# Kernel tuning notes

Hardware: AMD Instinct MI355X
Metric: run time of the kernel (lower is better)

Reference implementation:

```python
import jax, jax.numpy as jnp
import numpy as np

LN_EPS = 1e-12


def _layernorm(x, gamma, beta):
    mu = jnp.mean(x, axis=-1, keepdims=True)
    var = jnp.mean((x - mu) ** 2, axis=-1, keepdims=True)
    return (x - mu) * jax.lax.rsqrt(var + LN_EPS) * gamma + beta


def _gcn(x, node_emb, time_emb, wpool, bpool, ln_g, ln_b):
    # x: [B,N,C]; node_emb: [N,D]; time_emb: [D]
    e = _layernorm(node_emb + time_emb[None, :], ln_g, ln_b)          # [N,D] (dropout in eval = identity)
    adj = jax.nn.softmax(e @ e.T, axis=1)                             # [N,N] dynamic adjacency
    weights = jnp.einsum('nd,dkio->nkio', e, wpool)                   # [N,2,Cin,Cout] per-node weights
    bias = e @ bpool                                                  # [N,Cout]
    # supports = [I, adj]: identity support is just x itself
    x_g = jnp.stack([x, jnp.einsum('nm,bmc->bnc', adj, x)], axis=2)   # [B,N,2,Cin]
    return jnp.einsum('bnki,nkio->bno', x_g, weights) + bias          # [B,N,Cout]


def setup_inputs() -> dict:
    key = jax.random.key(0)
    ks = jax.random.split(key, 10)
    B, N, Cin, H, D = 32, 2048, 32, 64, 64
    s = 0.1
    return {
        'x': jax.random.normal(ks[0], (B, N, Cin), jnp.float32),
        'state': jax.random.normal(ks[1], (B, N, H), jnp.float32),
        'node_embeddings': jax.random.normal(ks[2], (N, D), jnp.float32),
        'time_embeddings': jax.random.normal(ks[3], (D,), jnp.float32),
        'gate_wpool': jax.random.normal(ks[4], (D, 2, Cin + H, 2 * H), jnp.float32) * s,
        'gate_bpool': jax.random.normal(ks[5], (D, 2 * H), jnp.float32) * s,
        'gate_ln_g': jnp.ones((D,), jnp.float32),
        'gate_ln_b': jnp.zeros((D,), jnp.float32),
        'update_wpool': jax.random.normal(ks[6], (D, 2, Cin + H, H), jnp.float32) * s,
        'update_bpool': jax.random.normal(ks[7], (D, H), jnp.float32) * s,
        'update_ln_g': jnp.ones((D,), jnp.float32),
        'update_ln_b': jnp.zeros((D,), jnp.float32),
    }


def reference(x, state, node_embeddings, time_embeddings,
              gate_wpool, gate_bpool, gate_ln_g, gate_ln_b,
              update_wpool, update_bpool, update_ln_g, update_ln_b):
    H = state.shape[-1]
    inp = jnp.concatenate([x, state], axis=-1)                        # [B,N,Cin+H]
    z_r = jax.nn.sigmoid(_gcn(inp, node_embeddings, time_embeddings,
                              gate_wpool, gate_bpool, gate_ln_g, gate_ln_b))
    z, r = z_r[..., :H], z_r[..., H:]
    cand = jnp.concatenate([x, z * state], axis=-1)
    hc = jnp.tanh(_gcn(cand, node_embeddings, time_embeddings,
                       update_wpool, update_bpool, update_ln_g, update_ln_b))
    return r * state + (1.0 - r) * hc
```

## Files before the change

kernel.cpp:

```cpp
#include <hip/hip_runtime.h>

typedef _Float16 f16;
typedef _Float16 half8 __attribute__((ext_vector_type(8)));
typedef float f32x4 __attribute__((ext_vector_type(4)));

#define NN 2048
#define BB 32
#define CINC 32
#define HH 64
#define DD 64
#define C1 96
#define KI 192
#define OG 128
#define OU 64
#define WCG 24576
#define WCU 12288

#define XGI(n, ks, b, kk) (((((size_t)(n)) * 6 + (ks)) * BB + (b)) * 32 + (kk))

__device__ __forceinline__ f32x4 mfma16(half8 a, half8 b, f32x4 c) {
  return __builtin_amdgcn_mfma_f32_16x16x32_f16(a, b, c, 0, 0, 0);
}

typedef __attribute__((address_space(1))) const void* gas_t;
typedef __attribute__((address_space(3))) void* las_t;
__device__ __forceinline__ void gl_lds16(const void* g, void* l) {
  __builtin_amdgcn_global_load_lds((gas_t)g, (las_t)l, 16, 0, 0);
}

#define SWZ(row, kb) (((row) << 7) + ((kb) ^ (((row) & 7) << 4)))

__global__ __launch_bounds__(256) void k_ln_bias(
    const float* __restrict__ ne, const float* __restrict__ te,
    const float* __restrict__ gg, const float* __restrict__ gb,
    const float* __restrict__ ug, const float* __restrict__ ub,
    const float* __restrict__ gbp, const float* __restrict__ ubp,
    f16* __restrict__ egh, f16* __restrict__ euh,
    float* __restrict__ biasg, float* __restrict__ biasu) {
  __shared__ float esg[4][64];
  __shared__ float esu[4][64];
  int nl = threadIdx.x >> 6;
  int node = blockIdx.x * 4 + nl;
  int d = threadIdx.x & 63;
  float v = ne[node * DD + d] + te[d];
  float s = v;
  #pragma unroll
  for (int m = 1; m < 64; m <<= 1) s += __shfl_xor(s, m, 64);
  float mu = s * (1.f / 64.f);
  float df = v - mu;
  float q = df * df;
  #pragma unroll
  for (int m = 1; m < 64; m <<= 1) q += __shfl_xor(q, m, 64);
  float rs = rsqrtf(q * (1.f / 64.f) + 1e-12f);
  float base = df * rs;
  float a = base * gg[d] + gb[d];
  float b = base * ug[d] + ub[d];
  egh[node * DD + d] = (f16)a;
  euh[node * DD + d] = (f16)b;
  esg[nl][d] = a; esu[nl][d] = b;
  __syncthreads();
  #pragma unroll
  for (int i = 0; i < 3; ++i) {
    int u = i * 256 + threadIdx.x;
    int un = u / 192, oo = u % 192;
    int n2 = blockIdx.x * 4 + un;
    float acc = 0.f;
    if (oo < OG) {
      #pragma unroll 8
      for (int dd = 0; dd < 64; ++dd) acc += esg[un][dd] * gbp[dd * OG + oo];
      biasg[(size_t)n2 * OG + oo] = acc;
    } else {
      int o = oo - OG;
      #pragma unroll 8
      for (int dd = 0; dd < 64; ++dd) acc += esu[un][dd] * ubp[dd * OU + o];
      biasu[(size_t)n2 * OU + o] = acc;
    }
  }
}

__global__ __launch_bounds__(256) void k_wpool_t(const float* __restrict__ gwp,
                                                 const float* __restrict__ uwp,
                                                 f16* __restrict__ wtg,
                                                 f16* __restrict__ wtu) {
  const int upd = blockIdx.z;
  if (upd && blockIdx.y >= OU / 16) return;
  const float* wpool = upd ? uwp : gwp;
  f16* wt = upd ? wtu : wtg;
  const int O = upd ? OU : OG;
  __shared__ float tile[64][17];
  int ki = blockIdx.x;
  int o0 = blockIdx.y * 16;
  int t = threadIdx.x;
  const int ks = ki >> 5, kk = ki & 31;
  #pragma unroll
  for (int i = 0; i < 4; ++i) {
    int e2 = i * 256 + t;
    int d = e2 >> 4, o = e2 & 15;
    tile[d][o] = wpool[((size_t)d * KI + ki) * O + o0 + o];
  }
  __syncthreads();
  #pragma unroll
  for (int i = 0; i < 4; ++i) {
    int e2 = i * 256 + t;
    int o = e2 >> 6, d = e2 & 63;
    size_t row = ((size_t)ks * O + (o0 + o)) * 32 + kk;
    wt[row * DD + d] = (f16)tile[d][o];
  }
}

__global__ __launch_bounds__(256) void k_build_inp(const float* __restrict__ x,
                                                   const float* __restrict__ st,
                                                   f16* __restrict__ cm,
                                                   f16* __restrict__ xg,
                                                   f16* __restrict__ sth) {
  __shared__ f16 tile[96][66];
  int mb = blockIdx.x * 64;
  int b = blockIdx.y;
  int t = threadIdx.x;
  #pragma unroll
  for (int i = 0; i < 24; ++i) {
    int e2 = i * 256 + t;
    int m = e2 / 96, c = e2 % 96;
    float v = (c < CINC) ? x[((size_t)b * NN + mb + m) * CINC + c]
                         : st[((size_t)b * NN + mb + m) * HH + c - CINC];
    f16 h = (f16)v;
    tile[c][m] = h;
    xg[XGI(mb + m, c >> 5, b, c & 31)] = h;
    if (c >= CINC) sth[((size_t)b * NN + mb + m) * HH + c - CINC] = h;
  }
  __syncthreads();
  #pragma unroll
  for (int i = 0; i < 24; ++i) {
    int e2 = i * 256 + t;
    int c = e2 >> 6, m = e2 & 63;
    cm[((size_t)b * C1 + c) * NN + mb + m] = tile[c][m];
  }
}

__global__ __launch_bounds__(256) void k_transpose_zs(const f16* __restrict__ zs,
                                                      f16* __restrict__ cm) {
  __shared__ f16 tile[64][66];
  int mb = blockIdx.x * 64;
  int b = blockIdx.y;
  int t = threadIdx.x;
  #pragma unroll
  for (int i = 0; i < 16; ++i) {
    int e2 = i * 256 + t;
    int m = e2 >> 6, o = e2 & 63;
    tile[o][m] = zs[((size_t)b * NN + mb + m) * HH + o];
  }
  __syncthreads();
  #pragma unroll
  for (int i = 0; i < 16; ++i) {
    int e2 = i * 256 + t;
    int o = e2 >> 6, m = e2 & 63;
    cm[((size_t)b * C1 + CINC + o) * NN + mb + m] = tile[o][m];
  }
}

__global__ __launch_bounds__(256) void k_attn(const f16* __restrict__ eh,
                                              f16* __restrict__ adj) {
  const int r0 = blockIdx.x * 16;
  const int w = threadIdx.x >> 6, lane = threadIdx.x & 63;
  const int fr = lane & 15, fq = lane >> 4;
  __shared__ float pm[4][16], ps[4][16];
  __shared__ float fm[16], fs[16];
  const half8 a0 = *(const half8*)&eh[(size_t)(r0 + fr) * DD + fq * 8];
  const half8 a1 = *(const half8*)&eh[(size_t)(r0 + fr) * DD + 32 + fq * 8];
  float m[4], s[4];
  #pragma unroll
  for (int r = 0; r < 4; ++r) { m[r] = -3.0e38f; s[r] = 0.f; }
  for (int ct = 0; ct < 32; ++ct) {
    const int c0 = w * 512 + ct * 16;
    half8 b0 = *(const half8*)&eh[(size_t)(c0 + fr) * DD + fq * 8];
    half8 b1 = *(const half8*)&eh[(size_t)(c0 + fr) * DD + 32 + fq * 8];
    f32x4 d = mfma16(a0, b0, f32x4{0.f, 0.f, 0.f, 0.f});
    d = mfma16(a1, b1, d);
    #pragma unroll
    for (int r = 0; r < 4; ++r) {
      float mn = fmaxf(m[r], d[r]);
      s[r] = s[r] * __expf(m[r] - mn) + __expf(d[r] - mn);
      m[r] = mn;
    }
  }
  #pragma unroll
  for (int r = 0; r < 4; ++r) {
    #pragma unroll
    for (int mk = 1; mk < 16; mk <<= 1) {
      float mo = __shfl_xor(m[r], mk, 64);
      float so = __shfl_xor(s[r], mk, 64);
      float mn = fmaxf(m[r], mo);
      s[r] = s[r] * __expf(m[r] - mn) + so * __expf(mo - mn);
      m[r] = mn;
    }
  }
  if (fr == 0) {
    #pragma unroll
    for (int r = 0; r < 4; ++r) { pm[w][fq * 4 + r] = m[r]; ps[w][fq * 4 + r] = s[r]; }
  }
  __syncthreads();
  if (threadIdx.x < 16) {
    float M = -3.0e38f;
    #pragma unroll
    for (int i = 0; i < 4; ++i) M = fmaxf(M, pm[i][threadIdx.x]);
    float S = 0.f;
    #pragma unroll
    for (int i = 0; i < 4; ++i) S += ps[i][threadIdx.x] * __expf(pm[i][threadIdx.x] - M);
    fm[threadIdx.x] = M; fs[threadIdx.x] = 1.f / S;
  }
  __syncthreads();
  float Mr[4], Sr[4];
  #pragma unroll
  for (int r = 0; r < 4; ++r) { Mr[r] = fm[fq * 4 + r]; Sr[r] = fs[fq * 4 + r]; }
  for (int ct = 0; ct < 32; ++ct) {
    const int c0 = w * 512 + ct * 16;
    half8 b0 = *(const half8*)&eh[(size_t)(c0 + fr) * DD + fq * 8];
    half8 b1 = *(const half8*)&eh[(size_t)(c0 + fr) * DD + 32 + fq * 8];
    f32x4 d = mfma16(a0, b0, f32x4{0.f, 0.f, 0.f, 0.f});
    d = mfma16(a1, b1, d);
    #pragma unroll
    for (int r = 0; r < 4; ++r)
      adj[(size_t)(r0 + fq * 4 + r) * NN + c0 + fr] = (f16)(__expf(d[r] - Mr[r]) * Sr[r]);
  }
}

#define BM 64
#define BN 96

__global__ __launch_bounds__(256, 4) void k_gemm_xa(const f16* __restrict__ A,
                                                    const f16* __restrict__ Bm,
                                                    f16* __restrict__ xg) {
  const int orig = blockIdx.x;
  const int xcd = orig & 7, j = orig >> 3;
  const int nb = (j >> 2) * BM;
  const int by = (xcd << 2) + (j & 3);
  const int cb = by * BN;
  const int tid = threadIdx.x;
  const int w = tid >> 6, lane = tid & 63;
  const int wr = (w >> 1) * 32, wc = (w & 1) * 48;
  const int fr = lane & 15, fq = lane >> 4;

  const int arow = tid >> 3;
  const int acolb = ((tid & 7) * 16) ^ ((arow & 7) << 4);
  const char* asrc = (const char*)A + (size_t)(nb + arow) * (NN * 2) + acolb;
  const char* bsrc = (const char*)Bm + (size_t)(cb + arow) * (NN * 2) + acolb;

  __shared__ f16 Al[2][BM * 64];
  __shared__ f16 Bl[2][BN * 64];
  auto stage = [&](int buf, int kt) {
    const size_t ko = (size_t)kt * 2;
    char* ad = (char*)&Al[buf][0] + (w << 10);
    char* bd = (char*)&Bl[buf][0] + (w << 10);
    gl_lds16(asrc + ko, ad);
    gl_lds16(asrc + ko + (size_t)32 * (NN * 2), ad + 4096);
    gl_lds16(bsrc + ko, bd);
    gl_lds16(bsrc + ko + (size_t)32 * (NN * 2), bd + 4096);
    gl_lds16(bsrc + ko + (size_t)64 * (NN * 2), bd + 8192);
  };

  f32x4 acc[2][3] = {};
  stage(0, 0);
  for (int kt = 0; kt < NN; kt += 64) {
    const int cur = (kt >> 6) & 1;
    if (kt + 64 < NN) {
      stage(cur ^ 1, kt + 64);
      asm volatile("s_waitcnt vmcnt(5)" ::: "memory");
    } else {
      asm volatile("s_waitcnt vmcnt(0)" ::: "memory");
    }
    __builtin_amdgcn_sched_barrier(0);
    __builtin_amdgcn_s_barrier();
    const char* Ab = (const char*)&Al[cur][0];
    const char* Bb = (const char*)&Bl[cur][0];
    half8 af[2][2], bf[2][3];
    #pragma unroll
    for (int k0 = 0; k0 < 2; ++k0) {
      const int kb = k0 * 64 + fq * 16;
      #pragma unroll
      for (int mt = 0; mt < 2; ++mt)
        af[k0][mt] = *(const half8*)(Ab + SWZ(wr + mt * 16 + fr, kb));
      #pragma unroll
      for (int nt = 0; nt < 3; ++nt)
        bf[k0][nt] = *(const half8*)(Bb + SWZ(wc + nt * 16 + fr, kb));
    }
    asm volatile("s_waitcnt lgkmcnt(0)" ::: "memory");
    __builtin_amdgcn_sched_barrier(0);
    __builtin_amdgcn_s_barrier();
    #pragma unroll
    for (int k0 = 0; k0 < 2; ++k0)
      #pragma unroll
      for (int mt = 0; mt < 2; ++mt)
        #pragma unroll
        for (int nt = 0; nt < 3; ++nt)
          acc[mt][nt] = mfma16(af[k0][mt], bf[k0][nt], acc[mt][nt]);
  }
  #pragma unroll
  for (int mt = 0; mt < 2; ++mt)
    #pragma unroll
    for (int nt = 0; nt < 3; ++nt)
      #pragma unroll
      for (int r = 0; r < 4; ++r) {
        int n = nb + wr + mt * 16 + fq * 4 + r;
        int l = wc + nt * 16 + fr;
        xg[XGI(n, 3 + (l >> 5), by, l & 31)] = (f16)acc[mt][nt][r];
      }
}

__global__ __launch_bounds__(256) void k_gemm_w2(const f16* __restrict__ A,
                                                 const f16* __restrict__ B,
                                                 f16* __restrict__ W, int ncols) {
  __shared__ f16 Al[128 * 64];
  __shared__ f16 Bl[128 * 64];
  const int cb = blockIdx.x * 128;
  const int nb = blockIdx.y * 128;
  const int tid = threadIdx.x;
  const int w = tid >> 6, lane = tid & 63;
  const int wr = (w >> 1) * 64, wc = (w & 1) * 64;
  const int fr = lane & 15, fq = lane >> 4;
  const int arow = tid >> 3;
  const int acolb = ((tid & 7) * 16) ^ ((arow & 7) << 4);
  const char* asrc = (const char*)A + (size_t)(nb + arow) * 128 + acolb;
  const char* bsrc = (const char*)B + (size_t)(cb + arow) * 128 + acolb;
  char* ad = (char*)Al + (w << 10);
  char* bd = (char*)Bl + (w << 10);
  #pragma unroll
  for (int j = 0; j < 4; ++j) gl_lds16(asrc + (size_t)j * 32 * 128, ad + j * 4096);
  #pragma unroll
  for (int j = 0; j < 4; ++j) gl_lds16(bsrc + (size_t)j * 32 * 128, bd + j * 4096);
  __syncthreads();
  f32x4 acc[4][4] = {};
  #pragma unroll
  for (int k0 = 0; k0 < 2; ++k0) {
    const int kb = k0 * 64 + fq * 16;
    half8 af[4], bf[4];
    #pragma unroll
    for (int mt = 0; mt < 4; ++mt)
      af[mt] = *(const half8*)((const char*)Al + SWZ(wr + mt * 16 + fr, kb));
    #pragma unroll
    for (int nt = 0; nt < 4; ++nt)
      bf[nt] = *(const half8*)((const char*)Bl + SWZ(wc + nt * 16 + fr, kb));
    #pragma unroll
    for (int mt = 0; mt < 4; ++mt)
      #pragma unroll
      for (int nt = 0; nt < 4; ++nt)
        acc[mt][nt] = mfma16(af[mt], bf[nt], acc[mt][nt]);
  }
  #pragma unroll
  for (int mt = 0; mt < 4; ++mt)
    #pragma unroll
    for (int nt = 0; nt < 4; ++nt)
      #pragma unroll
      for (int r = 0; r < 4; ++r) {
        int n = nb + wr + mt * 16 + fq * 4 + r;
        int c = cb + wc + nt * 16 + fr;
        W[(size_t)n * ncols + c] = (f16)acc[mt][nt][r];
      }
}

template <bool GATE>
__global__ __launch_bounds__(256) void k_apply3(
    const f16* __restrict__ xg, const f16* __restrict__ W,
    const float* __restrict__ bias,
    const f16* __restrict__ sth,
    f16* xgw, f16* __restrict__ zs, f16* __restrict__ rbuf,
    float* __restrict__ outp) {
  constexpr int O = GATE ? OG : OU;
  constexpr int WS = GATE ? WCG : WCU;
  constexpr int NOT_ = GATE ? 2 : 1;
  const int n = blockIdx.x;
  const int lane = threadIdx.x & 63, w = threadIdx.x >> 6;
  const int fr = lane & 15, fq = lane >> 4;
  half8 af[2][6];
  #pragma unroll
  for (int mt = 0; mt < 2; ++mt) {
    #pragma unroll
    for (int ks = 0; ks < 6; ++ks)
      af[mt][ks] = *(const half8*)&xg[XGI(n, ks, mt * 16 + fr, fq * 8)];
  }
  if (GATE) __syncthreads();
  half8 bf[6][NOT_];
  #pragma unroll
  for (int ks = 0; ks < 6; ++ks) {
    #pragma unroll
    for (int ot = 0; ot < NOT_; ++ot) {
      int o = (GATE ? (w * 2 + ot) : w) * 16 + fr;
      bf[ks][ot] = *(const half8*)&W[(size_t)n * WS + (((size_t)ks * O + o) << 5) + fq * 8];
    }
  }
  f32x4 acc[2][NOT_] = {};
  #pragma unroll
  for (int ks = 0; ks < 6; ++ks)
    #pragma unroll
    for (int ot = 0; ot < NOT_; ++ot)
      #pragma unroll
      for (int mt = 0; mt < 2; ++mt)
        acc[mt][ot] = mfma16(af[mt][ks], bf[ks][ot], acc[mt][ot]);
  #pragma unroll
  for (int mt = 0; mt < 2; ++mt)
    #pragma unroll
    for (int ot = 0; ot < NOT_; ++ot) {
      const int o = (GATE ? (w * 2 + ot) : w) * 16 + fr;
      const float bs = bias[(size_t)n * O + o];
      #pragma unroll
      for (int r = 0; r < 4; ++r) {
        int b = mt * 16 + fq * 4 + r;
        float val = acc[mt][ot][r] + bs;
        if (GATE) {
          float s = 1.f / (1.f + expf(-val));
          if (o < HH) {
            size_t bno = ((size_t)b * NN + n) * HH + o;
            float zst = s * (float)sth[bno];
            xgw[XGI(n, 1 + (o >> 5), b, o & 31)] = (f16)zst;
            zs[bno] = (f16)zst;
          } else {
            rbuf[((size_t)b * NN + n) * HH + (o - HH)] = (f16)s;
          }
        } else {
          size_t bno = ((size_t)b * NN + n) * HH + o;
          float hc = tanhf(val);
          float rr = (float)rbuf[bno];
          outp[bno] = rr * (float)sth[bno] + (1.f - rr) * hc;
        }
      }
    }
}

extern "C" void kernel_launch(void* const* d_in, const int* in_sizes, int n_in,
                              void* d_out, int out_size, void* d_ws, size_t ws_size,
                              hipStream_t stream) {
  const float* x   = (const float*)d_in[0];
  const float* st  = (const float*)d_in[1];
  const float* ne  = (const float*)d_in[2];
  const float* te  = (const float*)d_in[3];
  const float* gwp = (const float*)d_in[4];
  const float* gbp = (const float*)d_in[5];
  const float* gg  = (const float*)d_in[6];
  const float* gb  = (const float*)d_in[7];
  const float* uwp = (const float*)d_in[8];
  const float* ubp = (const float*)d_in[9];
  const float* ug  = (const float*)d_in[10];
  const float* ub  = (const float*)d_in[11];
  float* out = (float*)d_out;

  char* wsb = (char*)d_ws;
  size_t off = 0;
  auto alloc = [&](size_t bytes) {
    char* p = wsb + off;
    off = (off + bytes + 255) & ~(size_t)255;
    return p;
  };
  f16*   egh   = (f16*)  alloc((size_t)NN * DD * 2);
  f16*   euh   = (f16*)  alloc((size_t)NN * DD * 2);
  float* biasg = (float*)alloc((size_t)NN * OG * 4);
  float* biasu = (float*)alloc((size_t)NN * OU * 4);
  f16*   wtg   = (f16*)  alloc((size_t)WCG * DD * 2);
  f16*   wtu   = (f16*)  alloc((size_t)WCU * DD * 2);
  f16*   xg    = (f16*)  alloc((size_t)NN * BB * KI * 2);
  f16*   cm    = (f16*)  alloc((size_t)BB * C1 * NN * 2);
  f16*   zs    = (f16*)  alloc((size_t)BB * NN * HH * 2);
  f16*   rbuf  = (f16*)  alloc((size_t)BB * NN * HH * 2);
  f16*   sth   = (f16*)  alloc((size_t)BB * NN * HH * 2);
  f16*   adj   = (f16*)  alloc((size_t)NN * NN * 2);
  f16*   W     = (f16*)  alloc((size_t)NN * WCG * 2);
  (void)ws_size; (void)in_sizes; (void)n_in; (void)out_size;

  hipLaunchKernelGGL(k_ln_bias, dim3(NN / 4), dim3(256), 0, stream,
                     ne, te, gg, gb, ug, ub, gbp, ubp,
                     egh, euh, biasg, biasu);
  hipLaunchKernelGGL(k_wpool_t, dim3(KI, OG / 16, 2), dim3(256), 0, stream,
                     gwp, uwp, wtg, wtu);
  hipLaunchKernelGGL(k_build_inp, dim3(NN / 64, BB), dim3(256), 0, stream,
                     x, st, cm, xg, sth);

  hipLaunchKernelGGL(k_attn, dim3(NN / 16), dim3(256), 0, stream, egh, adj);
  hipLaunchKernelGGL(k_gemm_xa, dim3(1024), dim3(256), 0, stream, adj, cm, xg);
  hipLaunchKernelGGL(k_gemm_w2, dim3(WCG / 128, NN / 128), dim3(256), 0, stream,
                     egh, wtg, W, WCG);
  hipLaunchKernelGGL((k_apply3<true>), dim3(NN), dim3(256), 0, stream,
                     xg, W, biasg, sth, xg, zs, rbuf, (float*)nullptr);
  hipLaunchKernelGGL(k_transpose_zs, dim3(NN / 64, BB), dim3(256), 0, stream, zs, cm);

  hipLaunchKernelGGL(k_attn, dim3(NN / 16), dim3(256), 0, stream, euh, adj);
  hipLaunchKernelGGL(k_gemm_xa, dim3(1024), dim3(256), 0, stream, adj, cm, xg);
  hipLaunchKernelGGL(k_gemm_w2, dim3(WCU / 128, NN / 128), dim3(256), 0, stream,
                     euh, wtu, W, WCU);
  hipLaunchKernelGGL((k_apply3<false>), dim3(NN), dim3(256), 0, stream,
                     xg, W, biasu, sth, (f16*)nullptr, (f16*)nullptr, rbuf, out);
}
```

Baseline: 222.5 us.

## Re-layout xg and per-node weights into 8-element segments and stage via LDS DMA

```diff
diff --git a/kernel.cpp b/kernel.cpp
--- a/kernel.cpp
+++ b/kernel.cpp
@@ -16,7 +16,8 @@
 #define WCG 24576
 #define WCU 12288
 
-#define XGI(n, ks, b, kk) (((((size_t)(n)) * 6 + (ks)) * BB + (b)) * 32 + (kk))
+#define XGI(n, ks, b, kk) \
+  ((((((size_t)(n)) * 6 + (ks)) * 4 + ((kk) >> 3)) * BB + (b)) * 8 + ((kk) & 7))
 
 __device__ __forceinline__ f32x4 mfma16(half8 a, half8 b, f32x4 c) {
   return __builtin_amdgcn_mfma_f32_16x16x32_f16(a, b, c, 0, 0, 0);
@@ -91,7 +92,8 @@
   int ki = blockIdx.x;
   int o0 = blockIdx.y * 16;
   int t = threadIdx.x;
-  const int ks = ki >> 5, kk = ki & 31;
+  const int seg = (ki >> 5) * 4 + ((ki >> 3) & 3);
+  const int kkl = ki & 7;
   #pragma unroll
   for (int i = 0; i < 4; ++i) {
     int e2 = i * 256 + t;
@@ -103,7 +105,7 @@
   for (int i = 0; i < 4; ++i) {
     int e2 = i * 256 + t;
     int o = e2 >> 6, d = e2 & 63;
-    size_t row = ((size_t)ks * O + (o0 + o)) * 32 + kk;
+    size_t row = ((size_t)seg * O + (o0 + o)) * 8 + kkl;
     wt[row * DD + d] = (f16)tile[d][o];
   }
 }
@@ -358,43 +360,47 @@
 }
 
 template <bool GATE>
-__global__ __launch_bounds__(256) void k_apply3(
+__global__ __launch_bounds__(256, GATE ? 2 : 4) void k_apply4(
     const f16* __restrict__ xg, const f16* __restrict__ W,
     const float* __restrict__ bias,
     const f16* __restrict__ sth,
     f16* xgw, f16* __restrict__ zs, f16* __restrict__ rbuf,
     float* __restrict__ outp) {
   constexpr int O = GATE ? OG : OU;
-  constexpr int WS = GATE ? WCG : WCU;
+  constexpr int WB = O * KI * 2;
+  constexpr int XB = KI * BB * 2;
   constexpr int NOT_ = GATE ? 2 : 1;
+  __shared__ __align__(128) char lds[WB + XB];
   const int n = blockIdx.x;
-  const int lane = threadIdx.x & 63, w = threadIdx.x >> 6;
+  const int tid = threadIdx.x;
+  const int w = tid >> 6, lane = tid & 63;
   const int fr = lane & 15, fq = lane >> 4;
-  half8 af[2][6];
-  #pragma unroll
-  for (int mt = 0; mt < 2; ++mt) {
-    #pragma unroll
-    for (int ks = 0; ks < 6; ++ks)
-      af[mt][ks] = *(const half8*)&xg[XGI(n, ks, mt * 16 + fr, fq * 8)];
-  }
-  if (GATE) __syncthreads();
-  half8 bf[6][NOT_];
+
+  const char* wsrc = (const char*)W + (size_t)n * WB + tid * 16;
+  const char* xsrc = (const char*)xg + (size_t)n * XB + tid * 16;
+  char* wdst = lds + (w << 10);
+  char* xdst = lds + WB + (w << 10);
+  #pragma unroll
+  for (int j = 0; j < WB / 4096; ++j) gl_lds16(wsrc + j * 4096, wdst + j * 4096);
+  #pragma unroll
+  for (int j = 0; j < XB / 4096; ++j) gl_lds16(xsrc + j * 4096, xdst + j * 4096);
+  __syncthreads();
+
+  const char* xl = lds + WB;
+  f32x4 acc[2][NOT_] = {};
   #pragma unroll
   for (int ks = 0; ks < 6; ++ks) {
+    const int seg = (ks * 4 + fq);
+    half8 af0 = *(const half8*)(xl + (seg * 32 + fr) * 16);
+    half8 af1 = *(const half8*)(xl + (seg * 32 + 16 + fr) * 16);
     #pragma unroll
     for (int ot = 0; ot < NOT_; ++ot) {
-      int o = (GATE ? (w * 2 + ot) : w) * 16 + fr;
-      bf[ks][ot] = *(const half8*)&W[(size_t)n * WS + (((size_t)ks * O + o) << 5) + fq * 8];
-    }
-  }
-  f32x4 acc[2][NOT_] = {};
-  #pragma unroll
-  for (int ks = 0; ks < 6; ++ks)
-    #pragma unroll
-    for (int ot = 0; ot < NOT_; ++ot)
-      #pragma unroll
-      for (int mt = 0; mt < 2; ++mt)
-        acc[mt][ot] = mfma16(af[mt][ks], bf[ks][ot], acc[mt][ot]);
+      const int o = (GATE ? (w * 2 + ot) : w) * 16 + fr;
+      half8 bf = *(const half8*)(lds + (seg * O + o) * 16);
+      acc[0][ot] = mfma16(af0, bf, acc[0][ot]);
+      acc[1][ot] = mfma16(af1, bf, acc[1][ot]);
+    }
+  }
   #pragma unroll
   for (int mt = 0; mt < 2; ++mt)
     #pragma unroll
@@ -476,7 +482,7 @@
   hipLaunchKernelGGL(k_gemm_xa, dim3(1024), dim3(256), 0, stream, adj, cm, xg);
   hipLaunchKernelGGL(k_gemm_w2, dim3(WCG / 128, NN / 128), dim3(256), 0, stream,
                      egh, wtg, W, WCG);
-  hipLaunchKernelGGL((k_apply3<true>), dim3(NN), dim3(256), 0, stream,
+  hipLaunchKernelGGL((k_apply4<true>), dim3(NN), dim3(256), 0, stream,
                      xg, W, biasg, sth, xg, zs, rbuf, (float*)nullptr);
   hipLaunchKernelGGL(k_transpose_zs, dim3(NN / 64, BB), dim3(256), 0, stream, zs, cm);
 
@@ -484,6 +490,6 @@
   hipLaunchKernelGGL(k_gemm_xa, dim3(1024), dim3(256), 0, stream, adj, cm, xg);
   hipLaunchKernelGGL(k_gemm_w2, dim3(WCU / 128, NN / 128), dim3(256), 0, stream,
                      euh, wtu, W, WCU);
-  hipLaunchKernelGGL((k_apply3<false>), dim3(NN), dim3(256), 0, stream,
+  hipLaunchKernelGGL((k_apply4<false>), dim3(NN), dim3(256), 0, stream,
                      xg, W, biasu, sth, (f16*)nullptr, (f16*)nullptr, rbuf, out);
 }
```

Measured after the change: 239.5 us. 1.08x slower.

## Merge prep kernels into one launch and batch both attention passes

Applied to the files above, without the earlier changes.

```diff
diff --git a/kernel.cpp b/kernel.cpp
--- a/kernel.cpp
+++ b/kernel.cpp
@@ -17,6 +17,7 @@
 #define WCU 12288
 
 #define XGI(n, ks, b, kk) (((((size_t)(n)) * 6 + (ks)) * BB + (b)) * 32 + (kk))
+#define STHI(n, b, o) ((((size_t)(n)) * BB + (b)) * HH + (o))
 
 __device__ __forceinline__ f32x4 mfma16(half8 a, half8 b, f32x4 c) {
   return __builtin_amdgcn_mfma_f32_16x16x32_f16(a, b, c, 0, 0, 0);
@@ -30,110 +31,108 @@
 
 #define SWZ(row, kb) (((row) << 7) + ((kb) ^ (((row) & 7) << 4)))
 
-__global__ __launch_bounds__(256) void k_ln_bias(
+__global__ __launch_bounds__(256) void k_prep(
     const float* __restrict__ ne, const float* __restrict__ te,
     const float* __restrict__ gg, const float* __restrict__ gb,
     const float* __restrict__ ug, const float* __restrict__ ub,
     const float* __restrict__ gbp, const float* __restrict__ ubp,
+    const float* __restrict__ gwp, const float* __restrict__ uwp,
+    const float* __restrict__ x, const float* __restrict__ st,
     f16* __restrict__ egh, f16* __restrict__ euh,
-    float* __restrict__ biasg, float* __restrict__ biasu) {
-  __shared__ float esg[4][64];
-  __shared__ float esu[4][64];
-  int nl = threadIdx.x >> 6;
-  int node = blockIdx.x * 4 + nl;
-  int d = threadIdx.x & 63;
-  float v = ne[node * DD + d] + te[d];
-  float s = v;
-  #pragma unroll
-  for (int m = 1; m < 64; m <<= 1) s += __shfl_xor(s, m, 64);
-  float mu = s * (1.f / 64.f);
-  float df = v - mu;
-  float q = df * df;
-  #pragma unroll
-  for (int m = 1; m < 64; m <<= 1) q += __shfl_xor(q, m, 64);
-  float rs = rsqrtf(q * (1.f / 64.f) + 1e-12f);
-  float base = df * rs;
-  float a = base * gg[d] + gb[d];
-  float b = base * ug[d] + ub[d];
-  egh[node * DD + d] = (f16)a;
-  euh[node * DD + d] = (f16)b;
-  esg[nl][d] = a; esu[nl][d] = b;
-  __syncthreads();
-  #pragma unroll
-  for (int i = 0; i < 3; ++i) {
-    int u = i * 256 + threadIdx.x;
-    int un = u / 192, oo = u % 192;
-    int n2 = blockIdx.x * 4 + un;
-    float acc = 0.f;
-    if (oo < OG) {
-      #pragma unroll 8
-      for (int dd = 0; dd < 64; ++dd) acc += esg[un][dd] * gbp[dd * OG + oo];
-      biasg[(size_t)n2 * OG + oo] = acc;
-    } else {
-      int o = oo - OG;
-      #pragma unroll 8
-      for (int dd = 0; dd < 64; ++dd) acc += esu[un][dd] * ubp[dd * OU + o];
-      biasu[(size_t)n2 * OU + o] = acc;
-    }
-  }
-}
-
-__global__ __launch_bounds__(256) void k_wpool_t(const float* __restrict__ gwp,
-                                                 const float* __restrict__ uwp,
-                                                 f16* __restrict__ wtg,
-                                                 f16* __restrict__ wtu) {
-  const int upd = blockIdx.z;
-  if (upd && blockIdx.y >= OU / 16) return;
-  const float* wpool = upd ? uwp : gwp;
-  f16* wt = upd ? wtu : wtg;
-  const int O = upd ? OU : OG;
-  __shared__ float tile[64][17];
-  int ki = blockIdx.x;
-  int o0 = blockIdx.y * 16;
-  int t = threadIdx.x;
-  const int ks = ki >> 5, kk = ki & 31;
-  #pragma unroll
-  for (int i = 0; i < 4; ++i) {
-    int e2 = i * 256 + t;
-    int d = e2 >> 4, o = e2 & 15;
-    tile[d][o] = wpool[((size_t)d * KI + ki) * O + o0 + o];
-  }
-  __syncthreads();
-  #pragma unroll
-  for (int i = 0; i < 4; ++i) {
-    int e2 = i * 256 + t;
-    int o = e2 >> 6, d = e2 & 63;
-    size_t row = ((size_t)ks * O + (o0 + o)) * 32 + kk;
-    wt[row * DD + d] = (f16)tile[d][o];
-  }
-}
-
-__global__ __launch_bounds__(256) void k_build_inp(const float* __restrict__ x,
-                                                   const float* __restrict__ st,
-                                                   f16* __restrict__ cm,
-                                                   f16* __restrict__ xg,
-                                                   f16* __restrict__ sth) {
-  __shared__ f16 tile[96][66];
-  int mb = blockIdx.x * 64;
-  int b = blockIdx.y;
-  int t = threadIdx.x;
-  #pragma unroll
-  for (int i = 0; i < 24; ++i) {
-    int e2 = i * 256 + t;
-    int m = e2 / 96, c = e2 % 96;
-    float v = (c < CINC) ? x[((size_t)b * NN + mb + m) * CINC + c]
-                         : st[((size_t)b * NN + mb + m) * HH + c - CINC];
-    f16 h = (f16)v;
-    tile[c][m] = h;
-    xg[XGI(mb + m, c >> 5, b, c & 31)] = h;
-    if (c >= CINC) sth[((size_t)b * NN + mb + m) * HH + c - CINC] = h;
-  }
-  __syncthreads();
-  #pragma unroll
-  for (int i = 0; i < 24; ++i) {
-    int e2 = i * 256 + t;
-    int c = e2 >> 6, m = e2 & 63;
-    cm[((size_t)b * C1 + c) * NN + mb + m] = tile[c][m];
+    float* __restrict__ biasg, float* __restrict__ biasu,
+    f16* __restrict__ wtg, f16* __restrict__ wtu,
+    f16* __restrict__ cm, f16* __restrict__ xg, f16* __restrict__ sth) {
+  __shared__ __align__(16) char smem[12672];
+  const int bid = blockIdx.x;
+  const int t = threadIdx.x;
+  if (bid < 512) {
+    float (*esg)[64] = (float(*)[64])smem;
+    float (*esu)[64] = (float(*)[64])(smem + 1024);
+    int nl = t >> 6;
+    int node = bid * 4 + nl;
+    int d = t & 63;
+    float v = ne[node * DD + d] + te[d];
+    float s = v;
+    #pragma unroll
+    for (int m = 1; m < 64; m <<= 1) s += __shfl_xor(s, m, 64);
+    float mu = s * (1.f / 64.f);
+    float df = v - mu;
+    float q = df * df;
+    #pragma unroll
+    for (int m = 1; m < 64; m <<= 1) q += __shfl_xor(q, m, 64);
+    float rs = rsqrtf(q * (1.f / 64.f) + 1e-12f);
+    float base = df * rs;
+    float a = base * gg[d] + gb[d];
+    float b = base * ug[d] + ub[d];
+    egh[node * DD + d] = (f16)a;
+    euh[node * DD + d] = (f16)b;
+    esg[nl][d] = a; esu[nl][d] = b;
+    __syncthreads();
+    #pragma unroll
+    for (int i = 0; i < 3; ++i) {
+      int u = i * 256 + t;
+      int un = u / 192, oo = u % 192;
+      int n2 = bid * 4 + un;
+      float acc = 0.f;
+      if (oo < OG) {
+        #pragma unroll 8
+        for (int dd = 0; dd < 64; ++dd) acc += esg[un][dd] * gbp[dd * OG + oo];
+        biasg[(size_t)n2 * OG + oo] = acc;
+      } else {
+        int o = oo - OG;
+        #pragma unroll 8
+        for (int dd = 0; dd < 64; ++dd) acc += esu[un][dd] * ubp[dd * OU + o];
+        biasu[(size_t)n2 * OU + o] = acc;
+      }
+    }
+  } else if (bid < 512 + 2304) {
+    float (*tile)[17] = (float(*)[17])smem;
+    const int t2 = bid - 512;
+    const int ki = t2 % 192;
+    const int oy = t2 / 192;
+    const int upd = oy >= 8;
+    const float* wpool = upd ? uwp : gwp;
+    f16* wt = upd ? wtu : wtg;
+    const int O = upd ? OU : OG;
+    const int o0 = (upd ? oy - 8 : oy) * 16;
+    const int ks = ki >> 5, kk = ki & 31;
+    #pragma unroll
+    for (int i = 0; i < 4; ++i) {
+      int e2 = i * 256 + t;
+      int d = e2 >> 4, o = e2 & 15;
+      tile[d][o] = wpool[((size_t)d * KI + ki) * O + o0 + o];
+    }
+    __syncthreads();
+    #pragma unroll
+    for (int i = 0; i < 4; ++i) {
+      int e2 = i * 256 + t;
+      int o = e2 >> 6, d = e2 & 63;
+      size_t row = ((size_t)ks * O + (o0 + o)) * 32 + kk;
+      wt[row * DD + d] = (f16)tile[d][o];
+    }
+  } else {
+    f16 (*tile)[66] = (f16(*)[66])smem;
+    const int t2 = bid - 2816;
+    const int mb = (t2 & 31) * 64;
+    const int b = t2 >> 5;
+    #pragma unroll
+    for (int i = 0; i < 24; ++i) {
+      int e2 = i * 256 + t;
+      int m = e2 / 96, c = e2 % 96;
+      float v = (c < CINC) ? x[((size_t)b * NN + mb + m) * CINC + c]
+                           : st[((size_t)b * NN + mb + m) * HH + c - CINC];
+      f16 h = (f16)v;
+      tile[c][m] = h;
+      xg[XGI(mb + m, c >> 5, b, c & 31)] = h;
+      if (c >= CINC) sth[STHI(mb + m, b, c - CINC)] = h;
+    }
+    __syncthreads();
+    #pragma unroll
+    for (int i = 0; i < 24; ++i) {
+      int e2 = i * 256 + t;
+      int c = e2 >> 6, m = e2 & 63;
+      cm[((size_t)b * C1 + c) * NN + mb + m] = tile[c][m];
+    }
   }
 }
 
@@ -158,8 +157,12 @@
   }
 }
 
-__global__ __launch_bounds__(256) void k_attn(const f16* __restrict__ eh,
-                                              f16* __restrict__ adj) {
+__global__ __launch_bounds__(256) void k_attn(const f16* __restrict__ eg,
+                                              const f16* __restrict__ eu,
+                                              f16* __restrict__ adjg,
+                                              f16* __restrict__ adju) {
+  const f16* eh = blockIdx.y ? eu : eg;
+  f16* adj = blockIdx.y ? adju : adjg;
   const int r0 = blockIdx.x * 16;
   const int w = threadIdx.x >> 6, lane = threadIdx.x & 63;
   const int fr = lane & 15, fq = lane >> 4;
@@ -378,23 +381,17 @@
       af[mt][ks] = *(const half8*)&xg[XGI(n, ks, mt * 16 + fr, fq * 8)];
   }
   if (GATE) __syncthreads();
-  half8 bf[6][NOT_];
+  f32x4 acc[2][NOT_] = {};
   #pragma unroll
   for (int ks = 0; ks < 6; ++ks) {
     #pragma unroll
     for (int ot = 0; ot < NOT_; ++ot) {
       int o = (GATE ? (w * 2 + ot) : w) * 16 + fr;
-      bf[ks][ot] = *(const half8*)&W[(size_t)n * WS + (((size_t)ks * O + o) << 5) + fq * 8];
-    }
-  }
-  f32x4 acc[2][NOT_] = {};
-  #pragma unroll
-  for (int ks = 0; ks < 6; ++ks)
-    #pragma unroll
-    for (int ot = 0; ot < NOT_; ++ot)
-      #pragma unroll
-      for (int mt = 0; mt < 2; ++mt)
-        acc[mt][ot] = mfma16(af[mt][ks], bf[ks][ot], acc[mt][ot]);
+      half8 bf = *(const half8*)&W[(size_t)n * WS + (((size_t)ks * O + o) << 5) + fq * 8];
+      #pragma unroll
+      for (int mt = 0; mt < 2; ++mt) acc[mt][ot] = mfma16(af[mt][ks], bf, acc[mt][ot]);
+    }
+  }
   #pragma unroll
   for (int mt = 0; mt < 2; ++mt)
     #pragma unroll
@@ -408,18 +405,17 @@
         if (GATE) {
           float s = 1.f / (1.f + expf(-val));
           if (o < HH) {
-            size_t bno = ((size_t)b * NN + n) * HH + o;
-            float zst = s * (float)sth[bno];
+            float zst = s * (float)sth[STHI(n, b, o)];
             xgw[XGI(n, 1 + (o >> 5), b, o & 31)] = (f16)zst;
-            zs[bno] = (f16)zst;
+            zs[((size_t)b * NN + n) * HH + o] = (f16)zst;
           } else {
-            rbuf[((size_t)b * NN + n) * HH + (o - HH)] = (f16)s;
+            rbuf[STHI(n, b, o - HH)] = (f16)s;
           }
         } else {
-          size_t bno = ((size_t)b * NN + n) * HH + o;
           float hc = tanhf(val);
-          float rr = (float)rbuf[bno];
-          outp[bno] = rr * (float)sth[bno] + (1.f - rr) * hc;
+          float rr = (float)rbuf[STHI(n, b, o)];
+          outp[((size_t)b * NN + n) * HH + o] =
+              rr * (float)sth[STHI(n, b, o)] + (1.f - rr) * hc;
         }
       }
     }
@@ -461,18 +457,16 @@
   f16*   rbuf  = (f16*)  alloc((size_t)BB * NN * HH * 2);
   f16*   sth   = (f16*)  alloc((size_t)BB * NN * HH * 2);
   f16*   adj   = (f16*)  alloc((size_t)NN * NN * 2);
+  f16*   adju  = (f16*)  alloc((size_t)NN * NN * 2);
   f16*   W     = (f16*)  alloc((size_t)NN * WCG * 2);
   (void)ws_size; (void)in_sizes; (void)n_in; (void)out_size;
 
-  hipLaunchKernelGGL(k_ln_bias, dim3(NN / 4), dim3(256), 0, stream,
-                     ne, te, gg, gb, ug, ub, gbp, ubp,
-                     egh, euh, biasg, biasu);
-  hipLaunchKernelGGL(k_wpool_t, dim3(KI, OG / 16, 2), dim3(256), 0, stream,
-                     gwp, uwp, wtg, wtu);
-  hipLaunchKernelGGL(k_build_inp, dim3(NN / 64, BB), dim3(256), 0, stream,
-                     x, st, cm, xg, sth);
-
-  hipLaunchKernelGGL(k_attn, dim3(NN / 16), dim3(256), 0, stream, egh, adj);
+  hipLaunchKernelGGL(k_prep, dim3(512 + 2304 + 1024), dim3(256), 0, stream,
+                     ne, te, gg, gb, ug, ub, gbp, ubp, gwp, uwp, x, st,
+                     egh, euh, biasg, biasu, wtg, wtu, cm, xg, sth);
+  hipLaunchKernelGGL(k_attn, dim3(NN / 16, 2), dim3(256), 0, stream,
+                     egh, euh, adj, adju);
+
   hipLaunchKernelGGL(k_gemm_xa, dim3(1024), dim3(256), 0, stream, adj, cm, xg);
   hipLaunchKernelGGL(k_gemm_w2, dim3(WCG / 128, NN / 128), dim3(256), 0, stream,
                      egh, wtg, W, WCG);
@@ -480,8 +474,7 @@
                      xg, W, biasg, sth, xg, zs, rbuf, (float*)nullptr);
   hipLaunchKernelGGL(k_transpose_zs, dim3(NN / 64, BB), dim3(256), 0, stream, zs, cm);
 
-  hipLaunchKernelGGL(k_attn, dim3(NN / 16), dim3(256), 0, stream, euh, adj);
-  hipLaunchKernelGGL(k_gemm_xa, dim3(1024), dim3(256), 0, stream, adj, cm, xg);
+  hipLaunchKernelGGL(k_gemm_xa, dim3(1024), dim3(256), 0, stream, adju, cm, xg);
   hipLaunchKernelGGL(k_gemm_w2, dim3(WCU / 128, NN / 128), dim3(256), 0, stream,
                      euh, wtu, W, WCU);
   hipLaunchKernelGGL((k_apply3<false>), dim3(NN), dim3(256), 0, stream,
```

Result: faster. 194.8 us, median of 2 (-12.4%).
